# Kernel tuning notes

Measured on AMD Instinct MI355X. Metric: run time of the kernel, lower is better.

Reference implementation:

```python
import jax, jax.numpy as jnp
import numpy as np

N_NODES = 50000
N_EDGES = 800000
D_IN = 128
D_OUT = 128


def setup_inputs() -> dict:
    key = jax.random.key(0)
    k1, k2, k3, k4, k5 = jax.random.split(key, 5)
    feature = jax.random.normal(k1, (N_NODES, D_IN), dtype=jnp.float32)
    src = jax.random.randint(k2, (N_EDGES,), 0, N_NODES, dtype=jnp.int32)
    dst = jax.random.randint(k3, (N_EDGES,), 0, N_NODES, dtype=jnp.int32)
    # nn.Linear-style init: U(-1/sqrt(in), 1/sqrt(in))
    bound = 1.0 / np.sqrt(D_IN)
    W = jax.random.uniform(k4, (D_OUT, D_IN), minval=-bound, maxval=bound, dtype=jnp.float32)
    b = jax.random.uniform(k5, (D_OUT,), minval=-bound, maxval=bound, dtype=jnp.float32)
    return {"feature": feature, "src": src, "dst": dst, "W": W, "b": b}


def reference(feature, src, dst, W, b):
    # copy_src: gather source node features along edges, then sum-reduce per dst
    msgs = feature[src]                                    # [E, D_IN]
    h = jax.ops.segment_sum(msgs, dst, num_segments=N_NODES)  # [N, D_IN]
    # linear projection: h @ W^T + b
    return jnp.einsum("nd,od->no", h, W) + b               # [N, D_OUT]
```

## Files before the change

kernel.cpp:

```cpp
#include <hip/hip_runtime.h>
#include <hip/hip_bf16.h>


#define BKT_SHIFT 6
#define MAX_BKT   800
#define NPART     128
#define CAP       1280
#define NCAP      64

typedef __attribute__((ext_vector_type(8))) short short8;
typedef __attribute__((ext_vector_type(4))) float float4v;

__device__ __forceinline__ unsigned short f2bf_rne(float f) {
    unsigned int u = __float_as_uint(f);
    u += 0x7FFFu + ((u >> 16) & 1u);
    return (unsigned short)(u >> 16);
}

__global__ __launch_bounds__(512) void conv_scatter_kernel(
    const float* __restrict__ feat, const float* __restrict__ W,
    unsigned short* __restrict__ out_bf, long nf, long nw,
    const int* __restrict__ src, const int* __restrict__ dst,
    int* __restrict__ cursor, unsigned int* __restrict__ pairs,
    int n_edges, int nb, int chunk)
{
    if ((int)blockIdx.x < NPART) {
        __shared__ int lcnt[MAX_BKT];
        __shared__ int lcur[MAX_BKT];
        int tid = threadIdx.x;
        int p   = blockIdx.x;
        int e0  = p * chunk;
        int e1  = min(e0 + chunk, n_edges);
        int cnt = e1 - e0;
        int nfull = cnt >> 2;

        for (int i = tid; i < nb; i += 512) lcnt[i] = 0;
        __syncthreads();
        for (int k = tid; k < nfull; k += 512) {
            int4 d4 = *(const int4*)(dst + e0 + k * 4);
            atomicAdd(&lcnt[d4.x >> BKT_SHIFT], 1);
            atomicAdd(&lcnt[d4.y >> BKT_SHIFT], 1);
            atomicAdd(&lcnt[d4.z >> BKT_SHIFT], 1);
            atomicAdd(&lcnt[d4.w >> BKT_SHIFT], 1);
        }
        for (int e = e0 + nfull * 4 + tid; e < e1; e += 512)
            atomicAdd(&lcnt[dst[e] >> BKT_SHIFT], 1);
        __syncthreads();
        for (int i = tid; i < nb; i += 512) {
            int c = lcnt[i];
            int base = c ? atomicAdd(&cursor[i], c) : 0;
            lcur[i] = i * CAP + base;
        }
        __syncthreads();
        for (int k = tid; k < nfull; k += 512) {
            int4 d4 = *(const int4*)(dst + e0 + k * 4);
            int4 s4 = *(const int4*)(src + e0 + k * 4);
            int p0 = atomicAdd(&lcur[d4.x >> BKT_SHIFT], 1);
            pairs[p0] = ((unsigned)(d4.x & 63) << 20) | (unsigned)s4.x;
            int p1 = atomicAdd(&lcur[d4.y >> BKT_SHIFT], 1);
            pairs[p1] = ((unsigned)(d4.y & 63) << 20) | (unsigned)s4.y;
            int p2 = atomicAdd(&lcur[d4.z >> BKT_SHIFT], 1);
            pairs[p2] = ((unsigned)(d4.z & 63) << 20) | (unsigned)s4.z;
            int p3 = atomicAdd(&lcur[d4.w >> BKT_SHIFT], 1);
            pairs[p3] = ((unsigned)(d4.w & 63) << 20) | (unsigned)s4.w;
        }
        for (int e = e0 + nfull * 4 + tid; e < e1; e += 512) {
            int d = dst[e];
            int pos = atomicAdd(&lcur[d >> BKT_SHIFT], 1);
            pairs[pos] = ((unsigned)(d & 63) << 20) | (unsigned)src[e];
        }
    } else {
        long i4 = ((long)(blockIdx.x - NPART) * 512 + threadIdx.x) * 4;
        if (i4 >= nf + nw) return;
        const float* srcp = (i4 < nf) ? (feat + i4) : (W + (i4 - nf));
        float4 v = *(const float4*)srcp;
        ushort4 o;
        o.x = f2bf_rne(v.x); o.y = f2bf_rne(v.y);
        o.z = f2bf_rne(v.z); o.w = f2bf_rne(v.w);
        *(ushort4*)(out_bf + i4) = o;
    }
}

#define HT_STRIDE 136

#define ACC8(U)                                                     \
    do {                                                            \
        acc[0] += __uint_as_float((U).x << 16);                     \
        acc[1] += __uint_as_float((U).x & 0xFFFF0000u);             \
        acc[2] += __uint_as_float((U).y << 16);                     \
        acc[3] += __uint_as_float((U).y & 0xFFFF0000u);             \
        acc[4] += __uint_as_float((U).z << 16);                     \
        acc[5] += __uint_as_float((U).z & 0xFFFF0000u);             \
        acc[6] += __uint_as_float((U).w << 16);                     \
        acc[7] += __uint_as_float((U).w & 0xFFFF0000u);             \
    } while (0)

__global__ __launch_bounds__(1024, 8) void gcn_gather_mm_kernel(
    const unsigned short* __restrict__ feat_bf,
    const unsigned int* __restrict__ pairs, const int* __restrict__ cursor,
    const unsigned short* __restrict__ w_bf, const float* __restrict__ bias,
    float* __restrict__ out, int n_nodes)
{
    __shared__ unsigned short htile[64 * HT_STRIDE];
    __shared__ int lstT[64][NCAP];
    __shared__ int lcnt[64];

    int tid   = threadIdx.x;
    int lane  = tid & 63;
    int w     = tid >> 6;
    int node0 = blockIdx.x << 6;
    int sub   = lane >> 4;
    int c16   = lane & 15;

    int bucket = blockIdx.x;
    int bstart = bucket * CAP;
    int bcnt   = min(cursor[bucket], CAP);

    ((int4*)lstT)[tid] = (int4){0, 0, 0, 0};
    if (tid < 64) lcnt[tid] = 0;
    __syncthreads();
    for (int i = tid; i < bcnt; i += 1024) {
        unsigned int pr = pairs[bstart + i];
        int local = (int)(pr >> 20);
        int pos = atomicAdd(&lcnt[local], 1);
        if (pos < NCAP) lstT[local][((pos & 3) << 4) | (pos >> 2)] = (int)(pr & 0xFFFFFu);
    }
    __syncthreads();

    const unsigned short* colp = feat_bf + c16 * 8;

    #pragma unroll
    for (int i = 0; i < 4; i++) {
        int loc = (w << 2) + i;
        float acc[8];
        #pragma unroll
        for (int j = 0; j < 8; j++) acc[j] = 0.f;

        int deg = (node0 + loc < n_nodes) ? min(lcnt[loc], NCAP) : 0;
        if (deg > 0) {
            int G = (deg + 15) >> 4;
            const int* tr = &lstT[loc][sub << 4];
            int4 s = *(const int4*)tr;
            for (int g = 0; g < G; ++g) {
                int4 snext;
                if (g + 1 < G) snext = *(const int4*)(tr + ((g + 1) << 2));
                uint4 ua = *(const uint4*)(colp + (size_t)s.x * 128);
                uint4 ub = *(const uint4*)(colp + (size_t)s.y * 128);
                uint4 uc = *(const uint4*)(colp + (size_t)s.z * 128);
                uint4 ud = *(const uint4*)(colp + (size_t)s.w * 128);
                int r0 = (g << 4) + sub;
                if (r0      < deg) ACC8(ua);
                if (r0 + 4  < deg) ACC8(ub);
                if (r0 + 8  < deg) ACC8(uc);
                if (r0 + 12 < deg) ACC8(ud);
                s = snext;
            }
            #pragma unroll
            for (int j = 0; j < 8; j++) {
                acc[j] += __shfl_xor(acc[j], 16);
                acc[j] += __shfl_xor(acc[j], 32);
            }
        }

        if (sub == 0) {
            short8 o;
            #pragma unroll
            for (int j = 0; j < 8; j++) o[j] = (short)f2bf_rne(acc[j]);
            *(short8*)(htile + loc * HT_STRIDE + c16 * 8) = o;
        }
    }

    __syncthreads();

    int m = lane & 15;
    int q = lane >> 4;

    #pragma unroll
    for (int pp = w; pp < 32; pp += 16) {
        int mt = pp >> 3;
        int nt = pp & 7;

        float4v accd = {0.f, 0.f, 0.f, 0.f};
        #pragma unroll
        for (int kk = 0; kk < 4; kk++) {
            short8 afrag = *(const short8*)(htile + (mt * 16 + m) * HT_STRIDE + kk * 32 + q * 8);
            short8 bfrag = *(const short8*)(w_bf + (size_t)(nt * 16 + m) * 128 + kk * 32 + q * 8);
            accd = __builtin_amdgcn_mfma_f32_16x16x32_bf16(afrag, bfrag, accd, 0, 0, 0);
        }
        float bv = bias[nt * 16 + m];
        #pragma unroll
        for (int r = 0; r < 4; r++) {
            int row = node0 + mt * 16 + q * 4 + r;
            if (row < n_nodes)
                out[(size_t)row * 128 + nt * 16 + m] = accd[r] + bv;
        }
    }
}

extern "C" void kernel_launch(void* const* d_in, const int* in_sizes, int n_in,
                              void* d_out, int out_size, void* d_ws, size_t ws_size,
                              hipStream_t stream) {
    const float* feature = (const float*)d_in[0];
    const int*   src     = (const int*)d_in[1];
    const int*   dst     = (const int*)d_in[2];
    const float* W       = (const float*)d_in[3];
    const float* b       = (const float*)d_in[4];

    const int D  = 128;
    int n_nodes  = in_sizes[0] / D;
    int n_edges  = in_sizes[1];
    int nb       = (n_nodes + 63) >> BKT_SHIFT;

    float* out = (float*)d_out;

    long nf = (long)n_nodes * D;
    long nw = (long)D * D;

    unsigned short* bf_base    = (unsigned short*)d_ws;
    unsigned short* feature_bf = bf_base;
    unsigned short* w_bf       = bf_base + nf;
    unsigned int* pairs  = (unsigned int*)(bf_base + nf + nw);
    int*          cursor = (int*)(pairs + (size_t)nb * CAP);

    int chunk = (n_edges + NPART - 1) / NPART;

    hipMemsetAsync(cursor, 0, (size_t)nb * sizeof(int), stream);

    {
        long conv_blocks = ((nf + nw) / 4 + 511) / 512;
        int grid = NPART + (int)conv_blocks;
        conv_scatter_kernel<<<grid, 512, 0, stream>>>(
            feature, W, bf_base, nf, nw, src, dst, cursor, pairs,
            n_edges, nb, chunk);
    }

    {
        gcn_gather_mm_kernel<<<nb, 1024, 0, stream>>>(
            feature_bf, pairs, cursor, w_bf, b, out, n_nodes);
    }
}
```

Baseline: 134.7 us.

## Scatter edges directly into per-node global adjacency lists via global atomics

Drops the two-pass bucket binning (local histogram, global cursor reservation, then per-bucket pair lists) and instead has each edge atomically take a slot in a per-node global counter, writing its source index straight into a fixed 64-slot per-node list in the interleaved layout. The gather kernel then reads neighbor indices directly from global memory with prefetch instead of rebuilding lists in shared memory. This removes a histogram pass, shared-memory list construction and a barrier. The cost is 800K scattered global atomics and scattered 4-byte writes. Unwritten slots hold garbage, so indices are masked to 17 bits to keep the loads in bounds.

```diff
diff --git a/kernel.cpp b/kernel.cpp
--- a/kernel.cpp
+++ b/kernel.cpp
@@ -2,11 +2,9 @@
 #include <hip/hip_bf16.h>
 
 
-#define BKT_SHIFT 6
-#define MAX_BKT   800
 #define NPART     128
-#define CAP       1280
 #define NCAP      64
+#define IDXMASK   0x1FFFFu
 
 typedef __attribute__((ext_vector_type(8))) short short8;
 typedef __attribute__((ext_vector_type(4))) float float4v;
@@ -21,53 +19,32 @@
     const float* __restrict__ feat, const float* __restrict__ W,
     unsigned short* __restrict__ out_bf, long nf, long nw,
     const int* __restrict__ src, const int* __restrict__ dst,
-    int* __restrict__ cursor, unsigned int* __restrict__ pairs,
-    int n_edges, int nb, int chunk)
+    unsigned int* __restrict__ ncur, int* __restrict__ lstT_g,
+    int n_edges, int chunk)
 {
     if ((int)blockIdx.x < NPART) {
-        __shared__ int lcnt[MAX_BKT];
-        __shared__ int lcur[MAX_BKT];
         int tid = threadIdx.x;
-        int p   = blockIdx.x;
-        int e0  = p * chunk;
+        int e0  = blockIdx.x * chunk;
         int e1  = min(e0 + chunk, n_edges);
         int cnt = e1 - e0;
         int nfull = cnt >> 2;
 
-        for (int i = tid; i < nb; i += 512) lcnt[i] = 0;
-        __syncthreads();
-        for (int k = tid; k < nfull; k += 512) {
-            int4 d4 = *(const int4*)(dst + e0 + k * 4);
-            atomicAdd(&lcnt[d4.x >> BKT_SHIFT], 1);
-            atomicAdd(&lcnt[d4.y >> BKT_SHIFT], 1);
-            atomicAdd(&lcnt[d4.z >> BKT_SHIFT], 1);
-            atomicAdd(&lcnt[d4.w >> BKT_SHIFT], 1);
-        }
-        for (int e = e0 + nfull * 4 + tid; e < e1; e += 512)
-            atomicAdd(&lcnt[dst[e] >> BKT_SHIFT], 1);
-        __syncthreads();
-        for (int i = tid; i < nb; i += 512) {
-            int c = lcnt[i];
-            int base = c ? atomicAdd(&cursor[i], c) : 0;
-            lcur[i] = i * CAP + base;
-        }
-        __syncthreads();
         for (int k = tid; k < nfull; k += 512) {
             int4 d4 = *(const int4*)(dst + e0 + k * 4);
             int4 s4 = *(const int4*)(src + e0 + k * 4);
-            int p0 = atomicAdd(&lcur[d4.x >> BKT_SHIFT], 1);
-            pairs[p0] = ((unsigned)(d4.x & 63) << 20) | (unsigned)s4.x;
-            int p1 = atomicAdd(&lcur[d4.y >> BKT_SHIFT], 1);
-            pairs[p1] = ((unsigned)(d4.y & 63) << 20) | (unsigned)s4.y;
-            int p2 = atomicAdd(&lcur[d4.z >> BKT_SHIFT], 1);
-            pairs[p2] = ((unsigned)(d4.z & 63) << 20) | (unsigned)s4.z;
-            int p3 = atomicAdd(&lcur[d4.w >> BKT_SHIFT], 1);
-            pairs[p3] = ((unsigned)(d4.w & 63) << 20) | (unsigned)s4.w;
+            unsigned t0 = atomicAdd(&ncur[d4.x], 1u);
+            if (t0 < NCAP) lstT_g[((size_t)d4.x << 6) | ((t0 & 3) << 4) | (t0 >> 2)] = s4.x;
+            unsigned t1 = atomicAdd(&ncur[d4.y], 1u);
+            if (t1 < NCAP) lstT_g[((size_t)d4.y << 6) | ((t1 & 3) << 4) | (t1 >> 2)] = s4.y;
+            unsigned t2 = atomicAdd(&ncur[d4.z], 1u);
+            if (t2 < NCAP) lstT_g[((size_t)d4.z << 6) | ((t2 & 3) << 4) | (t2 >> 2)] = s4.z;
+            unsigned t3 = atomicAdd(&ncur[d4.w], 1u);
+            if (t3 < NCAP) lstT_g[((size_t)d4.w << 6) | ((t3 & 3) << 4) | (t3 >> 2)] = s4.w;
         }
         for (int e = e0 + nfull * 4 + tid; e < e1; e += 512) {
             int d = dst[e];
-            int pos = atomicAdd(&lcur[d >> BKT_SHIFT], 1);
-            pairs[pos] = ((unsigned)(d & 63) << 20) | (unsigned)src[e];
+            unsigned t = atomicAdd(&ncur[d], 1u);
+            if (t < NCAP) lstT_g[((size_t)d << 6) | ((t & 3) << 4) | (t >> 2)] = src[e];
         }
     } else {
         long i4 = ((long)(blockIdx.x - NPART) * 512 + threadIdx.x) * 4;
@@ -97,12 +74,11 @@
 
 __global__ __launch_bounds__(1024, 8) void gcn_gather_mm_kernel(
     const unsigned short* __restrict__ feat_bf,
-    const unsigned int* __restrict__ pairs, const int* __restrict__ cursor,
+    const int* __restrict__ lstT_g, const unsigned int* __restrict__ ncur,
     const unsigned short* __restrict__ w_bf, const float* __restrict__ bias,
     float* __restrict__ out, int n_nodes)
 {
     __shared__ unsigned short htile[64 * HT_STRIDE];
-    __shared__ int lstT[64][NCAP];
     __shared__ int lcnt[64];
 
     int tid   = threadIdx.x;
@@ -112,42 +88,40 @@
     int sub   = lane >> 4;
     int c16   = lane & 15;
 
-    int bucket = blockIdx.x;
-    int bstart = bucket * CAP;
-    int bcnt   = min(cursor[bucket], CAP);
-
-    ((int4*)lstT)[tid] = (int4){0, 0, 0, 0};
-    if (tid < 64) lcnt[tid] = 0;
+    if (tid < 64) {
+        int node = node0 + tid;
+        lcnt[tid] = (node < n_nodes) ? min((int)ncur[node], NCAP) : 0;
+    }
     __syncthreads();
-    for (int i = tid; i < bcnt; i += 1024) {
-        unsigned int pr = pairs[bstart + i];
-        int local = (int)(pr >> 20);
-        int pos = atomicAdd(&lcnt[local], 1);
-        if (pos < NCAP) lstT[local][((pos & 3) << 4) | (pos >> 2)] = (int)(pr & 0xFFFFFu);
-    }
-    __syncthreads();
 
     const unsigned short* colp = feat_bf + c16 * 8;
+    int bl = w << 2;
+    const int* tr0 = lstT_g + (((size_t)(node0 + bl)) << 6) + (sub << 4);
+
+    int4 scur = *(const int4*)tr0;
 
     #pragma unroll
     for (int i = 0; i < 4; i++) {
-        int loc = (w << 2) + i;
+        const int* tr = tr0 + (i << 6);
+        int4 snode = scur;
+        if (i < 3) snode = *(const int4*)(tr + 64);
+
+        int loc = bl + i;
         float acc[8];
         #pragma unroll
         for (int j = 0; j < 8; j++) acc[j] = 0.f;
 
-        int deg = (node0 + loc < n_nodes) ? min(lcnt[loc], NCAP) : 0;
+        int deg = lcnt[loc];
         if (deg > 0) {
             int G = (deg + 15) >> 4;
-            const int* tr = &lstT[loc][sub << 4];
-            int4 s = *(const int4*)tr;
+            int4 s = scur;
             for (int g = 0; g < G; ++g) {
-                int4 snext;
+                int4 snext = s;
                 if (g + 1 < G) snext = *(const int4*)(tr + ((g + 1) << 2));
-                uint4 ua = *(const uint4*)(colp + (size_t)s.x * 128);
-                uint4 ub = *(const uint4*)(colp + (size_t)s.y * 128);
-                uint4 uc = *(const uint4*)(colp + (size_t)s.z * 128);
-                uint4 ud = *(const uint4*)(colp + (size_t)s.w * 128);
+                uint4 ua = *(const uint4*)(colp + (size_t)((unsigned)s.x & IDXMASK) * 128);
+                uint4 ub = *(const uint4*)(colp + (size_t)((unsigned)s.y & IDXMASK) * 128);
+                uint4 uc = *(const uint4*)(colp + (size_t)((unsigned)s.z & IDXMASK) * 128);
+                uint4 ud = *(const uint4*)(colp + (size_t)((unsigned)s.w & IDXMASK) * 128);
                 int r0 = (g << 4) + sub;
                 if (r0      < deg) ACC8(ua);
                 if (r0 + 4  < deg) ACC8(ub);
@@ -168,6 +142,7 @@
             for (int j = 0; j < 8; j++) o[j] = (short)f2bf_rne(acc[j]);
             *(short8*)(htile + loc * HT_STRIDE + c16 * 8) = o;
         }
+        scur = snode;
     }
 
     __syncthreads();
@@ -209,33 +184,34 @@
     const int D  = 128;
     int n_nodes  = in_sizes[0] / D;
     int n_edges  = in_sizes[1];
-    int nb       = (n_nodes + 63) >> BKT_SHIFT;
+    int nb       = (n_nodes + 63) >> 6;
 
     float* out = (float*)d_out;
 
     long nf = (long)n_nodes * D;
     long nw = (long)D * D;
+    long nn64 = (long)nb << 6;
 
     unsigned short* bf_base    = (unsigned short*)d_ws;
     unsigned short* feature_bf = bf_base;
     unsigned short* w_bf       = bf_base + nf;
-    unsigned int* pairs  = (unsigned int*)(bf_base + nf + nw);
-    int*          cursor = (int*)(pairs + (size_t)nb * CAP);
+    int*          lstT_g = (int*)(bf_base + nf + nw);
+    unsigned int* ncur   = (unsigned int*)(lstT_g + (size_t)nn64 * NCAP);
 
     int chunk = (n_edges + NPART - 1) / NPART;
 
-    hipMemsetAsync(cursor, 0, (size_t)nb * sizeof(int), stream);
+    hipMemsetAsync(ncur, 0, (size_t)n_nodes * sizeof(unsigned int), stream);
 
     {
         long conv_blocks = ((nf + nw) / 4 + 511) / 512;
         int grid = NPART + (int)conv_blocks;
         conv_scatter_kernel<<<grid, 512, 0, stream>>>(
-            feature, W, bf_base, nf, nw, src, dst, cursor, pairs,
-            n_edges, nb, chunk);
+            feature, W, bf_base, nf, nw, src, dst, ncur, lstT_g,
+            n_edges, chunk);
     }
 
     {
         gcn_gather_mm_kernel<<<nb, 1024, 0, stream>>>(
-            feature_bf, pairs, cursor, w_bf, b, out, n_nodes);
-    }
-}
+            feature_bf, lstT_g, ncur, w_bf, b, out, n_nodes);
+    }
+}
```

Result: slower. 169.9 us (+26.1%).
